# Performance work log

Hardware: AMD Instinct MI355X
Metric: run time of the kernel (lower is better)

Reference implementation:

```python
import jax, jax.numpy as jnp
import numpy as np

K = 5
PAD = K // 2
EPS = 1e-8  # torch cosine_similarity default eps


def setup_inputs() -> dict:
    key = jax.random.key(0)
    k1, k2 = jax.random.split(key)
    x = jax.random.normal(k1, (8, 64, 112, 112), dtype=jnp.float32)
    spatial_weight = jax.random.normal(k2, (K * K,), dtype=jnp.float32)
    return {"x": x, "spatial_weight": spatial_weight}


def _extract_patches(x):
    # x: (B, C, H, W) -> patches: (B, C, K*K, H, W), zero-padded neighborhood,
    # tap order row-major over (ki, kj) to match F.unfold's layout.
    B, C, H, W = x.shape
    xp = jnp.pad(x, ((0, 0), (0, 0), (PAD, PAD), (PAD, PAD)))
    taps = [xp[:, :, i:i + H, j:j + W] for i in range(K) for j in range(K)]
    return jnp.stack(taps, axis=2)


def reference(x, spatial_weight):
    # patches: (B, C, K2, H, W)
    patches = _extract_patches(x)
    # channel-wise dot between center pixel and each neighborhood tap
    dot = jnp.einsum('bchw,bckhw->bkhw', x, patches)          # (B, K2, H, W)
    norm_x = jnp.sqrt(jnp.sum(x * x, axis=1))                  # (B, H, W)
    norm_p = jnp.sqrt(jnp.sum(patches * patches, axis=1))      # (B, K2, H, W)
    sim = dot / jnp.maximum(norm_x[:, None] * norm_p, EPS)     # cosine sim
    likelihood = (sim + 1.0) * 0.5
    weight = likelihood * spatial_weight[None, :, None, None]  # (B, K2, H, W)
    out = jnp.einsum('bckhw,bkhw->bchw', patches, weight)      # (B, C, H, W)
    return out
```

## Files before the change

### kernel.cpp

```cpp
#include <hip/hip_runtime.h>


typedef _Float16 half8 __attribute__((ext_vector_type(8)));
typedef _Float16 half4 __attribute__((ext_vector_type(4)));
typedef _Float16 half2t __attribute__((ext_vector_type(2)));
typedef float f32x4 __attribute__((ext_vector_type(4)));
typedef float f32x2 __attribute__((ext_vector_type(2)));

constexpr int Cc = 64, Hc = 112, Wc = 112;
constexpr int HWc = Hc * Wc;
constexpr float EPSc = 1e-8f;
constexpr int TH = 8, TW = 8;
constexpr int WR = 12, HALO = 144;
constexpr int ST_2 = 160;
constexpr int ST_W = 96;
constexpr int NTX = 14;

__device__ __forceinline__ int idxt(int pos, int col) {
    return pos * 64 + (col ^ ((pos & 7) << 3));
}
__device__ __forceinline__ int idx2(int row, int col) {
    return (row * ST_2 + col) ^ ((row & 7) << 3);
}
__device__ __forceinline__ int idxw(int row, int col) {
    return (row * ST_W + col) ^ ((row & 7) << 3);
}

__global__ __launch_bounds__(256, 4) void cooc_mfma(
    const float* __restrict__ x, const float* __restrict__ swg,
    float* __restrict__ out)
{
    __shared__ __align__(16) _Float16 Hs_t[HALO * 64];
    __shared__ __align__(16) _Float16 Hs2[64 * ST_2];
    __shared__ float nxs[HALO];
    __shared__ float sws[25];
    _Float16* const Wt = Hs_t;

    const int t = threadIdx.x;
    const int wv = t >> 6, l = t & 63;
    const int lo16 = l & 15, hi4 = l >> 4;
    const int bid = blockIdx.x;
    const int b = bid & 7;
    const int tile = bid >> 3;
    const int th = tile / NTX, twi = tile - th * NTX;
    const int h0 = th * TH, w0 = twi * TW;
    const float* xb = x + (size_t)b * Cc * HWc;
    const half8 z8 = {0, 0, 0, 0, 0, 0, 0, 0};

    if (t < 128) {
        const int row = t >> 1, c8 = 144 + (t & 1) * 8;
        *(half8*)&Hs2[idx2(row, c8)] = z8;
    }
    if (t < 25) sws[t] = swg[t];

#pragma unroll
    for (int it = 0; it < 5; ++it) {
        const int task = t + it * 256;
        if (task < 1152) {
            const int cq = task / 72;
            const int pp = task - cq * 72;
            const int r_ = pp / 6, pc2 = (pp - r_ * 6) * 2;
            const int gh = h0 + r_ - 2, gw = w0 + pc2 - 2;
            const bool inb = ((unsigned)gh < (unsigned)Hc) && ((unsigned)gw < (unsigned)Wc);
            const int ch0 = cq * 4;
            const float* src = xb + (size_t)ch0 * HWc + gh * Wc + gw;
            f32x2 v0 = {0.f, 0.f}, v1 = v0, v2 = v0, v3 = v0;
            if (inb) {
                v0 = *(const f32x2*)(src);
                v1 = *(const f32x2*)(src + (size_t)1 * HWc);
                v2 = *(const f32x2*)(src + (size_t)2 * HWc);
                v3 = *(const f32x2*)(src + (size_t)3 * HWc);
            }
            const int pos0 = r_ * WR + pc2;
            const half4 hx = {(_Float16)v0.x, (_Float16)v1.x, (_Float16)v2.x, (_Float16)v3.x};
            const half4 hy = {(_Float16)v0.y, (_Float16)v1.y, (_Float16)v2.y, (_Float16)v3.y};
            *(half4*)&Hs_t[idxt(pos0, ch0)] = hx;
            *(half4*)&Hs_t[idxt(pos0 + 1, ch0)] = hy;
            const half2t p0 = {hx[0], hy[0]}, p1 = {hx[1], hy[1]};
            const half2t p2 = {hx[2], hy[2]}, p3 = {hx[3], hy[3]};
            *(half2t*)&Hs2[idx2(ch0 + 0, pos0)] = p0;
            *(half2t*)&Hs2[idx2(ch0 + 1, pos0)] = p1;
            *(half2t*)&Hs2[idx2(ch0 + 2, pos0)] = p2;
            *(half2t*)&Hs2[idx2(ch0 + 3, pos0)] = p3;
        }
    }
    __syncthreads();

    if (t < HALO) {
        float s = 0.f;
#pragma unroll
        for (int i = 0; i < 8; ++i) {
            const half8 h = *(const half8*)&Hs_t[idxt(t, i * 8)];
#pragma unroll
            for (int j = 0; j < 8; ++j) {
                const float f = (float)h[j];
                s = fmaf(f, f, s);
            }
        }
        nxs[t] = sqrtf(s);
    }

    const int p = wv * 16 + lo16;
    const int cpos = ((p >> 3) + 2) * WR + (p & 7) + 2;
    half8 bfr[2];
#pragma unroll
    for (int ks = 0; ks < 2; ++ks)
        bfr[ks] = *(const half8*)&Hs_t[idxt(cpos, ks * 32 + hi4 * 8)];

    const int mt_lo = (3 * wv) >> 1;
    f32x4 acc[5];
#pragma unroll
    for (int i = 0; i < 5; ++i) acc[i] = (f32x4){0.f, 0.f, 0.f, 0.f};
#pragma unroll
    for (int i = 0; i < 5; ++i) {
        const int q0 = (mt_lo + i) * 16 + lo16;
#pragma unroll
        for (int ks = 0; ks < 2; ++ks) {
            const half8 afr = *(const half8*)&Hs_t[idxt(q0, ks * 32 + hi4 * 8)];
            acc[i] = __builtin_amdgcn_mfma_f32_16x16x32_f16(afr, bfr[ks], acc[i], 0, 0, 0);
        }
    }

    half8 b2[5];
#pragma unroll
    for (int ks = 0; ks < 5; ++ks)
        b2[ks] = *(const half8*)&Hs2[idx2(wv * 16 + lo16, ks * 32 + hi4 * 8)];

    __syncthreads();

    {
        const int zc = (wv == 0 || wv == 3) ? 80 : 0;
        if (hi4 < 2) *(half8*)&Wt[idxw(p, zc + hi4 * 8)] = z8;

        const float nxp = nxs[cpos];
        const int W0 = ((3 * wv) >> 2) * 32;
        const int prw = p >> 3, pcl = p & 7;
#pragma unroll
        for (int i = 0; i < 5; ++i) {
            const int qb = (mt_lo + i) * 16 + hi4 * 4;
            _Float16 hw[4];
#pragma unroll
            for (int r = 0; r < 4; ++r) {
                const int q = qb + r;
                const int qr = q / WR, qc = q - qr * WR;
                const int ih = qr - prw, iw = qc - pcl;
                const float sv = ((unsigned)ih <= 4u && (unsigned)iw <= 4u)
                                     ? sws[ih * 5 + iw] : 0.f;
                const float denom = fmaxf(nxp * nxs[q], EPSc);
                const float sim = acc[i][r] / denom;
                hw[r] = (_Float16)((sim + 1.f) * 0.5f * sv);
            }
            const half4 w4 = {hw[0], hw[1], hw[2], hw[3]};
            *(half4*)&Wt[idxw(p, qb - W0)] = w4;
        }
    }
    __syncthreads();

    f32x4 acc2[4];
#pragma unroll
    for (int nt = 0; nt < 4; ++nt) acc2[nt] = (f32x4){0.f, 0.f, 0.f, 0.f};
#pragma unroll
    for (int nt = 0; nt < 4; ++nt) {
        const int ksl = (3 * nt) >> 2;
#pragma unroll
        for (int s = 0; s < 3; ++s) {
            const half8 wtf = *(const half8*)&Wt[idxw(nt * 16 + lo16, s * 32 + hi4 * 8)];
            acc2[nt] = __builtin_amdgcn_mfma_f32_16x16x32_f16(wtf, b2[ksl + s], acc2[nt], 0, 0, 0);
        }
    }

    {
        const int ch = wv * 16 + lo16;
        float* ochan = out + (size_t)b * Cc * HWc + (size_t)ch * HWc;
        const int pr_base = hi4 >> 1, pc0 = (hi4 & 1) * 4;
#pragma unroll
        for (int nt = 0; nt < 4; ++nt) {
            const int gh = h0 + 2 * nt + pr_base;
            *(f32x4*)&ochan[gh * Wc + w0 + pc0] = acc2[nt];
        }
    }
}

extern "C" void kernel_launch(void* const* d_in, const int* in_sizes, int n_in,
                              void* d_out, int out_size, void* d_ws, size_t ws_size,
                              hipStream_t stream) {
    const float* x = (const float*)d_in[0];
    const float* sw = (const float*)d_in[1];
    float* out = (float*)d_out;
    cooc_mfma<<<dim3(8 * NTX * NTX), dim3(256), 0, stream>>>(x, sw, out);
}
```

Before: 26.19 us.

## Process two tiles per block with register-prefetched second tile load

Result: slower. 44.10 us (+68.4%).

```diff
diff --git a/kernel.cpp b/kernel.cpp
--- a/kernel.cpp
+++ b/kernel.cpp
@@ -41,9 +41,11 @@
     const int lo16 = l & 15, hi4 = l >> 4;
     const int bid = blockIdx.x;
     const int b = bid & 7;
-    const int tile = bid >> 3;
-    const int th = tile / NTX, twi = tile - th * NTX;
-    const int h0 = th * TH, w0 = twi * TW;
+    const int pair = bid >> 3;
+    const int tile0 = pair * 2;
+    const int trow = tile0 / NTX;
+    const int h0 = trow * TH;
+    const int w00 = (tile0 - trow * NTX) * TW;
     const float* xb = x + (size_t)b * Cc * HWc;
     const half8 z8 = {0, 0, 0, 0, 0, 0, 0, 0};
 
@@ -53,130 +55,167 @@
     }
     if (t < 25) sws[t] = swg[t];
 
-#pragma unroll
-    for (int it = 0; it < 5; ++it) {
-        const int task = t + it * 256;
-        if (task < 1152) {
-            const int cq = task / 72;
-            const int pp = task - cq * 72;
-            const int r_ = pp / 6, pc2 = (pp - r_ * 6) * 2;
-            const int gh = h0 + r_ - 2, gw = w0 + pc2 - 2;
-            const bool inb = ((unsigned)gh < (unsigned)Hc) && ((unsigned)gw < (unsigned)Wc);
-            const int ch0 = cq * 4;
-            const float* src = xb + (size_t)ch0 * HWc + gh * Wc + gw;
-            f32x2 v0 = {0.f, 0.f}, v1 = v0, v2 = v0, v3 = v0;
-            if (inb) {
-                v0 = *(const f32x2*)(src);
-                v1 = *(const f32x2*)(src + (size_t)1 * HWc);
-                v2 = *(const f32x2*)(src + (size_t)2 * HWc);
-                v3 = *(const f32x2*)(src + (size_t)3 * HWc);
-            }
-            const int pos0 = r_ * WR + pc2;
-            const half4 hx = {(_Float16)v0.x, (_Float16)v1.x, (_Float16)v2.x, (_Float16)v3.x};
-            const half4 hy = {(_Float16)v0.y, (_Float16)v1.y, (_Float16)v2.y, (_Float16)v3.y};
-            *(half4*)&Hs_t[idxt(pos0, ch0)] = hx;
-            *(half4*)&Hs_t[idxt(pos0 + 1, ch0)] = hy;
-            const half2t p0 = {hx[0], hy[0]}, p1 = {hx[1], hy[1]};
-            const half2t p2 = {hx[2], hy[2]}, p3 = {hx[3], hy[3]};
-            *(half2t*)&Hs2[idx2(ch0 + 0, pos0)] = p0;
-            *(half2t*)&Hs2[idx2(ch0 + 1, pos0)] = p1;
-            *(half2t*)&Hs2[idx2(ch0 + 2, pos0)] = p2;
-            *(half2t*)&Hs2[idx2(ch0 + 3, pos0)] = p3;
-        }
-    }
-    __syncthreads();
-
-    if (t < HALO) {
-        float s = 0.f;
-#pragma unroll
-        for (int i = 0; i < 8; ++i) {
-            const half8 h = *(const half8*)&Hs_t[idxt(t, i * 8)];
-#pragma unroll
-            for (int j = 0; j < 8; ++j) {
-                const float f = (float)h[j];
-                s = fmaf(f, f, s);
-            }
-        }
-        nxs[t] = sqrtf(s);
-    }
+    f32x2 rg[5][4];
+
+    auto load_tile = [&](int w0) {
+#pragma unroll
+        for (int it = 0; it < 5; ++it) {
+            const int task = t + it * 256;
+            if (task < 1152) {
+                const int cq = task / 72;
+                const int pp = task - cq * 72;
+                const int r_ = pp / 6, pc2 = (pp - r_ * 6) * 2;
+                const int gh = h0 + r_ - 2, gw = w0 + pc2 - 2;
+                const bool inb = ((unsigned)gh < (unsigned)Hc) &&
+                                 ((unsigned)gw < (unsigned)Wc);
+                const float* src = xb + (size_t)(cq * 4) * HWc + gh * Wc + gw;
+                const f32x2 z = {0.f, 0.f};
+                f32x2 v0 = z, v1 = z, v2 = z, v3 = z;
+                if (inb) {
+                    v0 = *(const f32x2*)(src);
+                    v1 = *(const f32x2*)(src + (size_t)1 * HWc);
+                    v2 = *(const f32x2*)(src + (size_t)2 * HWc);
+                    v3 = *(const f32x2*)(src + (size_t)3 * HWc);
+                }
+                rg[it][0] = v0; rg[it][1] = v1; rg[it][2] = v2; rg[it][3] = v3;
+            }
+        }
+    };
+    auto write_tile = [&]() {
+#pragma unroll
+        for (int it = 0; it < 5; ++it) {
+            const int task = t + it * 256;
+            if (task < 1152) {
+                const int cq = task / 72;
+                const int pp = task - cq * 72;
+                const int r_ = pp / 6, pc2 = (pp - r_ * 6) * 2;
+                const int pos0 = r_ * WR + pc2, ch0 = cq * 4;
+                const f32x2 v0 = rg[it][0], v1 = rg[it][1];
+                const f32x2 v2 = rg[it][2], v3 = rg[it][3];
+                const half4 hx = {(_Float16)v0.x, (_Float16)v1.x,
+                                  (_Float16)v2.x, (_Float16)v3.x};
+                const half4 hy = {(_Float16)v0.y, (_Float16)v1.y,
+                                  (_Float16)v2.y, (_Float16)v3.y};
+                *(half4*)&Hs_t[idxt(pos0, ch0)] = hx;
+                *(half4*)&Hs_t[idxt(pos0 + 1, ch0)] = hy;
+                const half2t p0 = {hx[0], hy[0]}, p1 = {hx[1], hy[1]};
+                const half2t p2 = {hx[2], hy[2]}, p3 = {hx[3], hy[3]};
+                *(half2t*)&Hs2[idx2(ch0 + 0, pos0)] = p0;
+                *(half2t*)&Hs2[idx2(ch0 + 1, pos0)] = p1;
+                *(half2t*)&Hs2[idx2(ch0 + 2, pos0)] = p2;
+                *(half2t*)&Hs2[idx2(ch0 + 3, pos0)] = p3;
+            }
+        }
+    };
 
     const int p = wv * 16 + lo16;
     const int cpos = ((p >> 3) + 2) * WR + (p & 7) + 2;
-    half8 bfr[2];
-#pragma unroll
-    for (int ks = 0; ks < 2; ++ks)
-        bfr[ks] = *(const half8*)&Hs_t[idxt(cpos, ks * 32 + hi4 * 8)];
-
     const int mt_lo = (3 * wv) >> 1;
-    f32x4 acc[5];
-#pragma unroll
-    for (int i = 0; i < 5; ++i) acc[i] = (f32x4){0.f, 0.f, 0.f, 0.f};
-#pragma unroll
-    for (int i = 0; i < 5; ++i) {
-        const int q0 = (mt_lo + i) * 16 + lo16;
-#pragma unroll
-        for (int ks = 0; ks < 2; ++ks) {
-            const half8 afr = *(const half8*)&Hs_t[idxt(q0, ks * 32 + hi4 * 8)];
-            acc[i] = __builtin_amdgcn_mfma_f32_16x16x32_f16(afr, bfr[ks], acc[i], 0, 0, 0);
-        }
-    }
-
-    half8 b2[5];
-#pragma unroll
-    for (int ks = 0; ks < 5; ++ks)
-        b2[ks] = *(const half8*)&Hs2[idx2(wv * 16 + lo16, ks * 32 + hi4 * 8)];
-
+
+    load_tile(w00);
+    write_tile();
     __syncthreads();
 
-    {
-        const int zc = (wv == 0 || wv == 3) ? 80 : 0;
-        if (hi4 < 2) *(half8*)&Wt[idxw(p, zc + hi4 * 8)] = z8;
-
-        const float nxp = nxs[cpos];
-        const int W0 = ((3 * wv) >> 2) * 32;
-        const int prw = p >> 3, pcl = p & 7;
-#pragma unroll
-        for (int i = 0; i < 5; ++i) {
-            const int qb = (mt_lo + i) * 16 + hi4 * 4;
-            _Float16 hw[4];
-#pragma unroll
-            for (int r = 0; r < 4; ++r) {
-                const int q = qb + r;
-                const int qr = q / WR, qc = q - qr * WR;
-                const int ih = qr - prw, iw = qc - pcl;
-                const float sv = ((unsigned)ih <= 4u && (unsigned)iw <= 4u)
-                                     ? sws[ih * 5 + iw] : 0.f;
-                const float denom = fmaxf(nxp * nxs[q], EPSc);
-                const float sim = acc[i][r] / denom;
-                hw[r] = (_Float16)((sim + 1.f) * 0.5f * sv);
-            }
-            const half4 w4 = {hw[0], hw[1], hw[2], hw[3]};
-            *(half4*)&Wt[idxw(p, qb - W0)] = w4;
-        }
-    }
-    __syncthreads();
-
-    f32x4 acc2[4];
-#pragma unroll
-    for (int nt = 0; nt < 4; ++nt) acc2[nt] = (f32x4){0.f, 0.f, 0.f, 0.f};
-#pragma unroll
-    for (int nt = 0; nt < 4; ++nt) {
-        const int ksl = (3 * nt) >> 2;
-#pragma unroll
-        for (int s = 0; s < 3; ++s) {
-            const half8 wtf = *(const half8*)&Wt[idxw(nt * 16 + lo16, s * 32 + hi4 * 8)];
-            acc2[nt] = __builtin_amdgcn_mfma_f32_16x16x32_f16(wtf, b2[ksl + s], acc2[nt], 0, 0, 0);
-        }
-    }
-
-    {
-        const int ch = wv * 16 + lo16;
-        float* ochan = out + (size_t)b * Cc * HWc + (size_t)ch * HWc;
-        const int pr_base = hi4 >> 1, pc0 = (hi4 & 1) * 4;
+#pragma unroll
+    for (int i = 0; i < 2; ++i) {
+        const int w0 = w00 + i * TW;
+        if (i == 0) load_tile(w00 + TW);
+
+        if (t < HALO) {
+            float s = 0.f;
+#pragma unroll
+            for (int ii = 0; ii < 8; ++ii) {
+                const half8 h = *(const half8*)&Hs_t[idxt(t, ii * 8)];
+#pragma unroll
+                for (int j = 0; j < 8; ++j) {
+                    const float f = (float)h[j];
+                    s = fmaf(f, f, s);
+                }
+            }
+            nxs[t] = sqrtf(s);
+        }
+
+        half8 bfr[2];
+#pragma unroll
+        for (int ks = 0; ks < 2; ++ks)
+            bfr[ks] = *(const half8*)&Hs_t[idxt(cpos, ks * 32 + hi4 * 8)];
+
+        f32x4 acc[5];
+#pragma unroll
+        for (int ii = 0; ii < 5; ++ii) acc[ii] = (f32x4){0.f, 0.f, 0.f, 0.f};
+#pragma unroll
+        for (int ii = 0; ii < 5; ++ii) {
+            const int q0 = (mt_lo + ii) * 16 + lo16;
+#pragma unroll
+            for (int ks = 0; ks < 2; ++ks) {
+                const half8 afr = *(const half8*)&Hs_t[idxt(q0, ks * 32 + hi4 * 8)];
+                acc[ii] = __builtin_amdgcn_mfma_f32_16x16x32_f16(afr, bfr[ks], acc[ii], 0, 0, 0);
+            }
+        }
+
+        half8 b2[5];
+#pragma unroll
+        for (int ks = 0; ks < 5; ++ks)
+            b2[ks] = *(const half8*)&Hs2[idx2(wv * 16 + lo16, ks * 32 + hi4 * 8)];
+
+        __syncthreads();
+
+        {
+            const int zc = (wv == 0 || wv == 3) ? 80 : 0;
+            if (hi4 < 2) *(half8*)&Wt[idxw(p, zc + hi4 * 8)] = z8;
+
+            const float nxp = nxs[cpos];
+            const int W0 = ((3 * wv) >> 2) * 32;
+            const int prw = p >> 3, pcl = p & 7;
+#pragma unroll
+            for (int ii = 0; ii < 5; ++ii) {
+                const int qb = (mt_lo + ii) * 16 + hi4 * 4;
+                _Float16 hw[4];
+#pragma unroll
+                for (int r = 0; r < 4; ++r) {
+                    const int q = qb + r;
+                    const int qr = q / WR, qc = q - qr * WR;
+                    const int ih = qr - prw, iw = qc - pcl;
+                    const float sv = ((unsigned)ih <= 4u && (unsigned)iw <= 4u)
+                                         ? sws[ih * 5 + iw] : 0.f;
+                    const float denom = fmaxf(nxp * nxs[q], EPSc);
+                    const float sim = acc[ii][r] / denom;
+                    hw[r] = (_Float16)((sim + 1.f) * 0.5f * sv);
+                }
+                const half4 w4 = {hw[0], hw[1], hw[2], hw[3]};
+                *(half4*)&Wt[idxw(p, qb - W0)] = w4;
+            }
+        }
+        __syncthreads();
+
+        f32x4 acc2[4];
+#pragma unroll
+        for (int nt = 0; nt < 4; ++nt) acc2[nt] = (f32x4){0.f, 0.f, 0.f, 0.f};
 #pragma unroll
         for (int nt = 0; nt < 4; ++nt) {
-            const int gh = h0 + 2 * nt + pr_base;
-            *(f32x4*)&ochan[gh * Wc + w0 + pc0] = acc2[nt];
+            const int ksl = (3 * nt) >> 2;
+#pragma unroll
+            for (int s = 0; s < 3; ++s) {
+                const half8 wtf = *(const half8*)&Wt[idxw(nt * 16 + lo16, s * 32 + hi4 * 8)];
+                acc2[nt] = __builtin_amdgcn_mfma_f32_16x16x32_f16(wtf, b2[ksl + s], acc2[nt], 0, 0, 0);
+            }
+        }
+
+        {
+            const int ch = wv * 16 + lo16;
+            float* ochan = out + (size_t)b * Cc * HWc + (size_t)ch * HWc;
+            const int pr_base = hi4 >> 1, pc0 = (hi4 & 1) * 4;
+#pragma unroll
+            for (int nt = 0; nt < 4; ++nt) {
+                const int gh = h0 + 2 * nt + pr_base;
+                *(f32x4*)&ochan[gh * Wc + w0 + pc0] = acc2[nt];
+            }
+        }
+
+        if (i == 0) {
+            __syncthreads();
+            write_tile();
+            __syncthreads();
         }
     }
 }
@@ -187,5 +226,5 @@
     const float* x = (const float*)d_in[0];
     const float* sw = (const float*)d_in[1];
     float* out = (float*)d_out;
-    cooc_mfma<<<dim3(8 * NTX * NTX), dim3(256), 0, stream>>>(x, sw, out);
-}
+    cooc_mfma<<<dim3(8 * (NTX * NTX / 2)), dim3(256), 0, stream>>>(x, sw, out);
+}
```
